# Optimization experiments

Measured on AMD Instinct MI355X. Metric: run time of the kernel, lower is better.

## Reference

```python
import jax, jax.numpy as jnp
import numpy as np
from functools import partial

K = 10
ALPHA = 0.1
N_NODES = 100000
N_EDGES = 1600000
IN_C, HID_C, OUT_C = 512, 256, 64


def setup_inputs() -> dict:
    key = jax.random.key(0)
    k1, k2, k3, k4, k5 = jax.random.split(key, 5)
    x = jax.random.normal(k1, (N_NODES, IN_C), dtype=jnp.float32)
    edge_index = jax.random.randint(k2, (2, N_EDGES), 0, N_NODES, dtype=jnp.int64)
    # Linear params (torch Linear: y = x @ W.T + b), Kaiming-ish scale
    w1 = jax.random.normal(k3, (HID_C, IN_C), dtype=jnp.float32) / np.sqrt(IN_C)
    b1 = jnp.zeros((HID_C,), dtype=jnp.float32)
    w2 = jax.random.normal(k4, (OUT_C, HID_C), dtype=jnp.float32) / np.sqrt(HID_C)
    b2 = jnp.zeros((OUT_C,), dtype=jnp.float32)
    return {"x": x, "edge_index": edge_index, "w1": w1, "b1": b1, "w2": w2, "b2": b2}


def _gcn_norm(edge_index, num_nodes):
    # add self-loops, symmetric normalization: norm_e = d[src]^-1/2 * d[dst]^-1/2
    loops = jnp.arange(num_nodes, dtype=edge_index.dtype)
    src = jnp.concatenate([edge_index[0], loops])
    dst = jnp.concatenate([edge_index[1], loops])
    ones = jnp.ones_like(dst, dtype=jnp.float32)
    deg = jax.ops.segment_sum(ones, dst, num_segments=num_nodes)
    dinv = jnp.where(deg > 0, jax.lax.rsqrt(deg), 0.0)
    norm = dinv[src] * dinv[dst]
    return src, dst, norm


def reference(x, edge_index, w1, b1, w2, b2):
    # inference mode: dropout = identity
    h = jax.nn.relu(x @ w1.T + b1)
    h = h @ w2.T + b2  # [N, OUT_C]
    n = x.shape[0]
    src, dst, norm = _gcn_norm(edge_index, n)
    h0 = h

    def step(hcur, _):
        msg = hcur[src] * norm[:, None]                      # gather [E+N, C]
        agg = jax.ops.segment_sum(msg, dst, num_segments=n)  # scatter-add [N, C]
        return (1.0 - ALPHA) * agg + ALPHA * h0, None

    h, _ = jax.lax.scan(step, h, None, length=K)
    return h
```

## Files before the change

kernel.cpp:

```cpp
#include <hip/hip_runtime.h>
#include <hip/hip_bf16.h>

#define N_NODES 100000
#define N_EDGES 1600000
#define IN_C 512
#define HID_C 256
#define OUT_C 64
#define K_ITERS 10
#define ALPHA 0.1f

typedef float f32x4 __attribute__((ext_vector_type(4)));
typedef _Float16 f16;
typedef _Float16 f16x4 __attribute__((ext_vector_type(4)));
typedef _Float16 f16x8 __attribute__((ext_vector_type(8)));

#define MFMA16(a, b, c) __builtin_amdgcn_mfma_f32_16x16x32_f16((a), (b), (c), 0, 0, 0)

__device__ __forceinline__ void gload16(const void* g, void* l) {
    __builtin_amdgcn_global_load_lds(
        (const __attribute__((address_space(1))) unsigned int*)g,
        (__attribute__((address_space(3))) unsigned int*)l, 16, 0, 0);
}

__global__ void k_count(const int* __restrict__ ei, int* __restrict__ cnt, int E) {
    int e = blockIdx.x * blockDim.x + threadIdx.x;
    if (e < E) atomicAdd(&cnt[ei[E + e]], 1);
}

__global__ void k_dinv(const int* __restrict__ cnt, float* __restrict__ dinv, int n) {
    int i = blockIdx.x * blockDim.x + threadIdx.x;
    if (i < n) dinv[i] = rsqrtf((float)cnt[i] + 1.0f);
}

#define SCB 1024
__global__ __launch_bounds__(256) void k_scan1(const int* __restrict__ cnt,
                                               int* __restrict__ bsum, int n) {
    __shared__ int s[256];
    int b = blockIdx.x, t = threadIdx.x;
    int base = b * SCB + t * 4;
    int local = 0;
#pragma unroll
    for (int j = 0; j < 4; ++j) {
        int i = base + j;
        if (i < n) local += cnt[i];
    }
    s[t] = local;
    __syncthreads();
    for (int off = 1; off < 256; off <<= 1) {
        int u = (t >= off) ? s[t - off] : 0;
        __syncthreads();
        s[t] += u;
        __syncthreads();
    }
    if (t == 255) bsum[b] = s[255];
}

__global__ __launch_bounds__(128) void k_scan2(const int* __restrict__ bsum,
                                               int* __restrict__ boff, int G,
                                               int* __restrict__ row_ptr, int n, int total) {
    __shared__ int s[128];
    int t = threadIdx.x;
    int v = (t < G) ? bsum[t] : 0;
    s[t] = v;
    __syncthreads();
    for (int off = 1; off < 128; off <<= 1) {
        int u = (t >= off) ? s[t - off] : 0;
        __syncthreads();
        s[t] += u;
        __syncthreads();
    }
    if (t < G) boff[t] = s[t] - v;
    if (t == 0) row_ptr[n] = total;
}

__global__ __launch_bounds__(256) void k_scan3(const int* __restrict__ cnt,
                                               const int* __restrict__ boff,
                                               int* __restrict__ row_ptr,
                                               int* __restrict__ cursor, int n) {
    __shared__ int s[256];
    int b = blockIdx.x, t = threadIdx.x;
    int base = b * SCB + t * 4;
    int c4[4];
    int local = 0;
#pragma unroll
    for (int j = 0; j < 4; ++j) {
        int i = base + j;
        c4[j] = (i < n) ? cnt[i] : 0;
        local += c4[j];
    }
    s[t] = local;
    __syncthreads();
    for (int off = 1; off < 256; off <<= 1) {
        int u = (t >= off) ? s[t - off] : 0;
        __syncthreads();
        s[t] += u;
        __syncthreads();
    }
    int run = boff[b] + s[t] - local;
#pragma unroll
    for (int j = 0; j < 4; ++j) {
        int i = base + j;
        if (i < n) {
            row_ptr[i] = run;
            cursor[i] = run;
            run += c4[j];
        }
    }
}

__global__ void k_fill(const int* __restrict__ ei, const float* __restrict__ dinv,
                       int* __restrict__ cursor, int2* __restrict__ csr_pack, int E) {
    int e = blockIdx.x * blockDim.x + threadIdx.x;
    if (e < E) {
        int s = ei[e];
        int d = ei[E + e];
        int pos = atomicAdd(&cursor[d], 1);
        csr_pack[pos] = make_int2(s, __float_as_int(dinv[s] * dinv[d]));
    }
}

__global__ void k_cast(const float* __restrict__ in, f16* __restrict__ out, int n) {
    int i = blockIdx.x * blockDim.x + threadIdx.x;
    if (i < n) out[i] = (f16)in[i];
}

__global__ __launch_bounds__(256, 4) void k_mlp2(
    const float* __restrict__ x,
    const f16* __restrict__ w1h,
    const float* __restrict__ b1,
    const f16* __restrict__ w2h,
    const float* __restrict__ b2,
    f16* __restrict__ h016, f16* __restrict__ hcur16, int n) {
    __shared__ __align__(16) union {
        struct {
            f16 Ah[64 * 40];
            f16 Bh[256 * 32];
        } p1;
        struct {
            f16 Hh[64 * 264];
        } p2;
    } sm;

    const int tid = threadIdx.x;
    const int l = tid & 63;
    const int w = tid >> 6;
    const int lr = l & 15;
    const int kg = l >> 4;
    const int row0 = blockIdx.x * 64;

    const int r0 = tid >> 3, kk0 = (tid & 7) * 4;
    const int r1 = (tid + 256) >> 3, kk1 = (tid & 7) * 4;
    int gr0 = row0 + r0; if (gr0 >= n) gr0 = n - 1;
    int gr1 = row0 + r1; if (gr1 >= n) gr1 = n - 1;
    const float* xp0 = &x[(size_t)gr0 * IN_C + kk0];
    const float* xp1 = &x[(size_t)gr1 * IN_C + kk1];

    f32x4 acc[4][4];
#pragma unroll
    for (int m = 0; m < 4; ++m)
#pragma unroll
        for (int nf = 0; nf < 4; ++nf) acc[m][nf] = (f32x4)0.0f;

    float4 xv0 = *(const float4*)xp0;
    float4 xv1 = *(const float4*)xp1;

    for (int ks = 0; ks < 16; ++ks) {
        const int k0 = ks * 32;
#pragma unroll
        for (int i = 0; i < 4; ++i) {
            int slot = tid + 256 * i;
            int row = slot >> 2;
            int kc = (slot & 3) ^ ((row >> 1) & 3);
            size_t goff = (size_t)row * IN_C + k0 + kc * 8;
            int sbase = (w * 64 + 256 * i) * 8;
            gload16(w1h + goff, &sm.p1.Bh[sbase]);
        }
        {
            f16x4 h4;
            h4.x = (f16)xv0.x; h4.y = (f16)xv0.y; h4.z = (f16)xv0.z; h4.w = (f16)xv0.w;
            *(f16x4*)&sm.p1.Ah[r0 * 40 + kk0] = h4;
            h4.x = (f16)xv1.x; h4.y = (f16)xv1.y; h4.z = (f16)xv1.z; h4.w = (f16)xv1.w;
            *(f16x4*)&sm.p1.Ah[r1 * 40 + kk1] = h4;
        }
        __syncthreads();

        if (ks < 15) {
            xv0 = *(const float4*)(xp0 + k0 + 32);
            xv1 = *(const float4*)(xp1 + k0 + 32);
        }

        f16x8 ah[4], bh[4];
#pragma unroll
        for (int m = 0; m < 4; ++m)
            ah[m] = *(const f16x8*)&sm.p1.Ah[(m * 16 + lr) * 40 + kg * 8];
#pragma unroll
        for (int nf = 0; nf < 4; ++nf) {
            int row = w * 64 + nf * 16 + lr;
            int kc = kg ^ ((row >> 1) & 3);
            bh[nf] = *(const f16x8*)&sm.p1.Bh[row * 32 + kc * 8];
        }
#pragma unroll
        for (int m = 0; m < 4; ++m)
#pragma unroll
            for (int nf = 0; nf < 4; ++nf)
                acc[m][nf] = MFMA16(ah[m], bh[nf], acc[m][nf]);
        __syncthreads();
    }

#pragma unroll
    for (int m = 0; m < 4; ++m)
#pragma unroll
        for (int nf = 0; nf < 4; ++nf) {
            int col = w * 64 + nf * 16 + lr;
            float bb = b1[col];
#pragma unroll
            for (int r = 0; r < 4; ++r) {
                int row = m * 16 + kg * 4 + r;
                float hv = acc[m][nf][r] + bb;
                hv = fmaxf(hv, 0.0f);
                sm.p2.Hh[row * 264 + col] = (f16)hv;
            }
        }
    __syncthreads();

    f32x4 acc2[4];
#pragma unroll
    for (int m = 0; m < 4; ++m) acc2[m] = (f32x4)0.0f;
    const int col2 = w * 16 + lr;

#pragma unroll
    for (int k0 = 0; k0 < HID_C; k0 += 32) {
        f16x8 b2h = *(const f16x8*)&w2h[(size_t)col2 * HID_C + k0 + kg * 8];
#pragma unroll
        for (int m = 0; m < 4; ++m) {
            f16x8 a2h = *(const f16x8*)&sm.p2.Hh[(m * 16 + lr) * 264 + k0 + kg * 8];
            acc2[m] = MFMA16(a2h, b2h, acc2[m]);
        }
    }

    float bb2 = b2[col2];
#pragma unroll
    for (int m = 0; m < 4; ++m)
#pragma unroll
        for (int r = 0; r < 4; ++r) {
            int grow = row0 + m * 16 + kg * 4 + r;
            if (grow < n) {
                float vv = acc2[m][r] + bb2;
                size_t idx = (size_t)grow * OUT_C + col2;
                h016[idx] = (f16)vv;
                hcur16[idx] = (f16)vv;
            }
        }
}

__global__ __launch_bounds__(256) void k_prop16(const f16* __restrict__ hin,
                                                const f16* __restrict__ h016,
                                                f16* __restrict__ hout,
                                                float* __restrict__ dout,
                                                const int* __restrict__ row_ptr,
                                                const int2* __restrict__ csr_pack,
                                                const float* __restrict__ dinv,
                                                int n, int final_iter) {
    const int gwave = (blockIdx.x * blockDim.x + threadIdx.x) >> 6;
    const int lane = threadIdx.x & 63;
    const int g = lane >> 3;
    const int cl = lane & 7;

    int node_raw = gwave * 8 + g;
    bool node_valid = node_raw < n;
    int node = node_valid ? node_raw : (n - 1);

    int e0 = row_ptr[node], e1 = row_ptr[node + 1];
    int nb = (e1 - e0 + 7) >> 3;
    nb = max(nb, __shfl_xor(nb, 8));
    nb = max(nb, __shfl_xor(nb, 16));
    nb = max(nb, __shfl_xor(nb, 32));

    float a[8];
#pragma unroll
    for (int q = 0; q < 8; ++q) a[q] = 0.0f;
    const int gbase = g * 8;

    int2 meta = csr_pack[min(e0 + cl, N_EDGES - 1)];
    for (int b = 0; b < nb; ++b) {
        int mbase = e0 + b * 8;
        int2 meta_next = meta;
        if (b + 1 < nb) meta_next = csr_pack[min(mbase + 8 + cl, N_EDGES - 1)];
#pragma unroll
        for (int j = 0; j < 8; ++j) {
            int s = __shfl(meta.x, gbase + j);
            float wv = __int_as_float(__shfl(meta.y, gbase + j));
            if (mbase + j < e1) {
                f16x8 v = *(const f16x8*)&hin[(size_t)s * OUT_C + cl * 8];
#pragma unroll
                for (int q = 0; q < 8; ++q) a[q] += wv * (float)v[q];
            }
        }
        meta = meta_next;
    }

    float dv = dinv[node];
    float d2 = dv * dv;
    size_t idx = (size_t)node * OUT_C + cl * 8;
    f16x8 sv = *(const f16x8*)&hin[idx];
    f16x8 h0v = *(const f16x8*)&h016[idx];
    float r[8];
#pragma unroll
    for (int q = 0; q < 8; ++q)
        r[q] = (1.0f - ALPHA) * (a[q] + d2 * (float)sv[q]) + ALPHA * (float)h0v[q];

    if (node_valid) {
        f16x8 o;
#pragma unroll
        for (int q = 0; q < 8; ++q) o[q] = (f16)r[q];
        *(f16x8*)&hout[idx] = o;
        if (final_iter) {
            float4 o0 = make_float4(r[0], r[1], r[2], r[3]);
            float4 o1 = make_float4(r[4], r[5], r[6], r[7]);
            *(float4*)&dout[idx] = o0;
            *(float4*)&dout[idx + 4] = o1;
        }
    }
}

extern "C" void kernel_launch(void* const* d_in, const int* in_sizes, int n_in,
                              void* d_out, int out_size, void* d_ws, size_t ws_size,
                              hipStream_t stream) {
    const float* x  = (const float*)d_in[0];
    const int*   ei = (const int*)d_in[1];
    const float* w1 = (const float*)d_in[2];
    const float* b1 = (const float*)d_in[3];
    const float* w2 = (const float*)d_in[4];
    const float* b2 = (const float*)d_in[5];
    float* dout = (float*)d_out;

    const int N = N_NODES;
    const int E = N_EDGES;
    const int G = (N + SCB - 1) / SCB;

    f16*   h16A    = (f16*)d_ws;
    f16*   h16B    = h16A + (size_t)N * OUT_C;
    f16*   h016    = h16B + (size_t)N * OUT_C;
    int2*  csr_pack = (int2*)(h016 + (size_t)N * OUT_C);
    float* dinv    = (float*)(csr_pack + E);
    int*   cnt     = (int*)(dinv + N);
    int*   row_ptr = cnt + N;
    int*   cursor  = row_ptr + (N + 1);
    f16*   w1h     = (f16*)(cursor + N);
    f16*   w2h     = w1h + (size_t)HID_C * IN_C;
    int*   bsum    = (int*)(w2h + (size_t)OUT_C * HID_C);
    int*   boff    = bsum + 128;

    hipMemsetAsync(cnt, 0, (size_t)N * sizeof(int), stream);

    k_count<<<(E + 255) / 256, 256, 0, stream>>>(ei, cnt, E);
    k_dinv<<<(N + 255) / 256, 256, 0, stream>>>(cnt, dinv, N);
    k_scan1<<<G, 256, 0, stream>>>(cnt, bsum, N);
    k_scan2<<<1, 128, 0, stream>>>(bsum, boff, G, row_ptr, N, E);
    k_scan3<<<G, 256, 0, stream>>>(cnt, boff, row_ptr, cursor, N);
    k_fill<<<(E + 255) / 256, 256, 0, stream>>>(ei, dinv, cursor, csr_pack, E);

    k_cast<<<(HID_C * IN_C + 255) / 256, 256, 0, stream>>>(w1, w1h, HID_C * IN_C);
    k_cast<<<(OUT_C * HID_C + 255) / 256, 256, 0, stream>>>(w2, w2h, OUT_C * HID_C);

    k_mlp2<<<(N + 63) / 64, 256, 0, stream>>>(x, w1h, b1, w2h, b2, h016, h16A, N);

    const int pwaves = (N + 7) / 8;
    const int pblocks = (pwaves * 64 + 255) / 256;
    for (int it = 0; it < K_ITERS; ++it) {
        const f16* pin = (it & 1) ? h16B : h16A;
        f16* pout = (it & 1) ? h16A : h16B;
        k_prop16<<<pblocks, 256, 0, stream>>>(pin, h016, pout, dout, row_ptr,
                                              csr_pack, dinv, N,
                                              it == K_ITERS - 1 ? 1 : 0);
    }
}
```

Baseline: 629.1 us.

## Double-buffer LDS tiles in MLP GEMM to overlap loads with MFMA

Splits the A and B LDS tiles of the first MLP GEMM into two buffers. The next k-slice of W1 is issued via global_load_lds and x is prefetched into registers while MFMAs run on the current buffer, which removes one barrier per iteration. This is meant to hide global load latency behind compute. In exchange LDS use per block roughly doubles for the first phase and the occupancy hint drops from 4 to 3 blocks per CU.

```diff
diff --git a/kernel.cpp b/kernel.cpp
--- a/kernel.cpp
+++ b/kernel.cpp
@@ -124,7 +124,7 @@
     if (i < n) out[i] = (f16)in[i];
 }
 
-__global__ __launch_bounds__(256, 4) void k_mlp2(
+__global__ __launch_bounds__(256, 3) void k_mlp2(
     const float* __restrict__ x,
     const f16* __restrict__ w1h,
     const float* __restrict__ b1,
@@ -133,8 +133,8 @@
     f16* __restrict__ h016, f16* __restrict__ hcur16, int n) {
     __shared__ __align__(16) union {
         struct {
-            f16 Ah[64 * 40];
-            f16 Bh[256 * 32];
+            f16 Ah[2][64 * 40];
+            f16 Bh[2][256 * 32];
         } p1;
         struct {
             f16 Hh[64 * 264];
@@ -149,11 +149,20 @@
     const int row0 = blockIdx.x * 64;
 
     const int r0 = tid >> 3, kk0 = (tid & 7) * 4;
-    const int r1 = (tid + 256) >> 3, kk1 = (tid & 7) * 4;
+    const int r1 = (tid + 256) >> 3;
     int gr0 = row0 + r0; if (gr0 >= n) gr0 = n - 1;
     int gr1 = row0 + r1; if (gr1 >= n) gr1 = n - 1;
     const float* xp0 = &x[(size_t)gr0 * IN_C + kk0];
-    const float* xp1 = &x[(size_t)gr1 * IN_C + kk1];
+    const float* xp1 = &x[(size_t)gr1 * IN_C + kk0];
+
+    int brow[4], bkc[4], bsb[4];
+#pragma unroll
+    for (int i = 0; i < 4; ++i) {
+        int slot = tid + 256 * i;
+        brow[i] = slot >> 2;
+        bkc[i] = (slot & 3) ^ ((brow[i] >> 1) & 3);
+        bsb[i] = (w * 64 + 256 * i) * 8;
+    }
 
     f32x4 acc[4][4];
 #pragma unroll
@@ -161,49 +170,56 @@
 #pragma unroll
         for (int nf = 0; nf < 4; ++nf) acc[m][nf] = (f32x4)0.0f;
 
-    float4 xv0 = *(const float4*)xp0;
-    float4 xv1 = *(const float4*)xp1;
+    {
+        float4 v0 = *(const float4*)xp0;
+        float4 v1 = *(const float4*)xp1;
+#pragma unroll
+        for (int i = 0; i < 4; ++i)
+            gload16(w1h + (size_t)brow[i] * IN_C + bkc[i] * 8, &sm.p1.Bh[0][bsb[i]]);
+        f16x4 h4;
+        h4.x = (f16)v0.x; h4.y = (f16)v0.y; h4.z = (f16)v0.z; h4.w = (f16)v0.w;
+        *(f16x4*)&sm.p1.Ah[0][r0 * 40 + kk0] = h4;
+        h4.x = (f16)v1.x; h4.y = (f16)v1.y; h4.z = (f16)v1.z; h4.w = (f16)v1.w;
+        *(f16x4*)&sm.p1.Ah[0][r1 * 40 + kk0] = h4;
+    }
+    __syncthreads();
 
     for (int ks = 0; ks < 16; ++ks) {
-        const int k0 = ks * 32;
-#pragma unroll
-        for (int i = 0; i < 4; ++i) {
-            int slot = tid + 256 * i;
-            int row = slot >> 2;
-            int kc = (slot & 3) ^ ((row >> 1) & 3);
-            size_t goff = (size_t)row * IN_C + k0 + kc * 8;
-            int sbase = (w * 64 + 256 * i) * 8;
-            gload16(w1h + goff, &sm.p1.Bh[sbase]);
-        }
-        {
-            f16x4 h4;
-            h4.x = (f16)xv0.x; h4.y = (f16)xv0.y; h4.z = (f16)xv0.z; h4.w = (f16)xv0.w;
-            *(f16x4*)&sm.p1.Ah[r0 * 40 + kk0] = h4;
-            h4.x = (f16)xv1.x; h4.y = (f16)xv1.y; h4.z = (f16)xv1.z; h4.w = (f16)xv1.w;
-            *(f16x4*)&sm.p1.Ah[r1 * 40 + kk1] = h4;
-        }
-        __syncthreads();
-
+        const int cur = ks & 1;
+        float4 xv0, xv1;
         if (ks < 15) {
-            xv0 = *(const float4*)(xp0 + k0 + 32);
-            xv1 = *(const float4*)(xp1 + k0 + 32);
+            const int kn = (ks + 1) * 32;
+            xv0 = *(const float4*)(xp0 + kn);
+            xv1 = *(const float4*)(xp1 + kn);
+#pragma unroll
+            for (int i = 0; i < 4; ++i)
+                gload16(w1h + (size_t)brow[i] * IN_C + kn + bkc[i] * 8,
+                        &sm.p1.Bh[cur ^ 1][bsb[i]]);
         }
 
         f16x8 ah[4], bh[4];
 #pragma unroll
         for (int m = 0; m < 4; ++m)
-            ah[m] = *(const f16x8*)&sm.p1.Ah[(m * 16 + lr) * 40 + kg * 8];
+            ah[m] = *(const f16x8*)&sm.p1.Ah[cur][(m * 16 + lr) * 40 + kg * 8];
 #pragma unroll
         for (int nf = 0; nf < 4; ++nf) {
             int row = w * 64 + nf * 16 + lr;
             int kc = kg ^ ((row >> 1) & 3);
-            bh[nf] = *(const f16x8*)&sm.p1.Bh[row * 32 + kc * 8];
+            bh[nf] = *(const f16x8*)&sm.p1.Bh[cur][row * 32 + kc * 8];
         }
 #pragma unroll
         for (int m = 0; m < 4; ++m)
 #pragma unroll
             for (int nf = 0; nf < 4; ++nf)
                 acc[m][nf] = MFMA16(ah[m], bh[nf], acc[m][nf]);
+
+        if (ks < 15) {
+            f16x4 h4;
+            h4.x = (f16)xv0.x; h4.y = (f16)xv0.y; h4.z = (f16)xv0.z; h4.w = (f16)xv0.w;
+            *(f16x4*)&sm.p1.Ah[cur ^ 1][r0 * 40 + kk0] = h4;
+            h4.x = (f16)xv1.x; h4.y = (f16)xv1.y; h4.z = (f16)xv1.z; h4.w = (f16)xv1.w;
+            *(f16x4*)&sm.p1.Ah[cur ^ 1][r1 * 40 + kk0] = h4;
+        }
         __syncthreads();
     }
 
```

Measured after the change: 621.4 us. No clear change (-1.2%).
